# Kernel optimization log

Hardware: AMD Instinct MI355X
Metric: run time of the kernel (lower is better)

## Reference

```python
import jax, jax.numpy as jnp
import numpy as np

B, N, G = 32, 262144, 256


def setup_inputs() -> dict:
    key = jax.random.key(0)
    k1, k2, k3 = jax.random.split(key, 3)
    pr = jax.random.normal(k1, (B, N), dtype=jnp.float32)
    inp_means = jax.random.normal(k2, (B, G), dtype=jnp.float32)
    vr = jax.random.randint(k3, (B, N, 1), 0, G, dtype=jnp.int32)
    W = jnp.ones((2,), dtype=jnp.float32)  # hist_weight, ones initializer
    return {"pr": pr, "inp_means": inp_means, "vr": vr, "W": W}


def reference(pr, inp_means, vr, W):
    sg = jax.lax.stop_gradient
    G = inp_means.shape[1]
    v = jnp.squeeze(vr, -1)  # [B, N] int cluster ids (stop_gradient in orig; int anyway)
    p_sg = sg(pr)

    # Per-batch segmented min/max/sum/any over clusters (replaces python loop over g).
    def seg(p, psg, vi):
        mn = jnp.full((G,), jnp.inf, p.dtype).at[vi].min(psg)    # min(where(gidx, pr, inf))
        mx = jnp.full((G,), -jnp.inf, p.dtype).at[vi].max(psg)   # max(where(gidx, pr, -inf))
        sm = jnp.zeros((G,), p.dtype).at[vi].add(p)              # sum(where(gidx, pr, 0))
        any_ = jnp.zeros((G,), bool).at[vi].set(True)            # reduce_any(gidx)
        return mn, mx, sm, any_

    vmins, vmaxs, vsum, vany = jax.vmap(seg)(pr, p_sg, v)  # each [B, G]
    # Original divides sum by cast(any)->1.0 (or 0/0=nan -> 0), i.e. the group SUM.
    vmeans = jnp.where(vany, vsum, jnp.zeros((), pr.dtype))
    vmeans = (inp_means * W[0] + vmeans * W[1]) / (W[0] + W[1])

    no_scale = vmins == vmaxs  # [B, G]
    vmins_g = jnp.take_along_axis(jnp.where(no_scale, 0.0, vmins), v, axis=1)  # [B, N]
    vmaxs_g = jnp.take_along_axis(jnp.where(no_scale, 1.0, vmaxs), v, axis=1)  # [B, N]

    sort_ids = jnp.argsort(vmeans, axis=1)
    orig_ids = jnp.argsort(sort_ids, axis=1)  # inverse permutation
    vs = jnp.take_along_axis(vmeans, sort_ids, axis=1)  # [B, G]
    cd = jnp.concatenate([vs[:, :1], vs, vs[:, -1:] * 2], axis=1)  # [B, G+2]
    # conv1d with kernel ones(2)/c, VALID: out[i] = (cd[i] + cd[i+1]) / c
    f0 = (cd[:, :-2] + cd[:, 1:-1]) / 1.999  # conv(...)[:, :-1]
    f1 = (cd[:, 1:-1] + cd[:, 2:]) / 2.001   # conv(...)[:, 1:]
    f0 = jnp.take_along_axis(
        jnp.where(no_scale, 0.0, jnp.take_along_axis(f0, orig_ids, axis=1)), v, axis=1)
    f1 = jnp.take_along_axis(
        jnp.where(no_scale, 1.0, jnp.take_along_axis(f1, orig_ids, axis=1)), v, axis=1)

    tmp = (sg(pr) - sg(vmins_g)) / sg(vmaxs_g - vmins_g) * (f1 - f0) + f0  # [B, N]
    bad = jnp.isnan(tmp) | (tmp == 0.0)
    s = pr / jnp.where(bad, 1.0, tmp)  # safe denominator (grad-safe)
    scale = jnp.where(bad | jnp.isnan(s) | jnp.isinf(s), 0.0, s)
    return pr * scale
```

## Files before the change

kernel.cpp:

```cpp
#include <hip/hip_runtime.h>
#include <math.h>

#define NB 32
#define NN 262144
#define NG 256
#define NC 64
#define CH (NN/NC)
#define SC (CH/4)
#define CD 64
#define ELD (NN/CD)

__global__ __launch_bounds__(256) void k_count(const int* __restrict__ vr,
                                               unsigned long long* __restrict__ wcnt16,
                                               unsigned* __restrict__ gid32){
  __shared__ unsigned sc[4][NG];
  const int t    = threadIdx.x;
  const int lane = t & 63;
  const int w    = t >> 6;
  sc[0][t] = 0u; sc[1][t] = 0u; sc[2][t] = 0u; sc[3][t] = 0u;
  __syncthreads();

  const int b = blockIdx.x / NC;
  const int c = blockIdx.x % NC;
  const size_t base = (size_t)b*NN + (size_t)c*CH;
  const int4* v4 = (const int4*)(vr + base);

#pragma unroll
  for (int i = 0; i < 4; i++){
    int idx = w*256 + i*64 + lane;
    int4 v = v4[idx];
    atomicAdd(&sc[w][v.x], 1u);
    atomicAdd(&sc[w][v.y], 1u);
    atomicAdd(&sc[w][v.z], 1u);
    atomicAdd(&sc[w][v.w], 1u);
    gid32[(base >> 2) + idx] =
      (unsigned)v.x | ((unsigned)v.y << 8) | ((unsigned)v.z << 16) | ((unsigned)v.w << 24);
  }
  __syncthreads();

  unsigned c0 = sc[0][t], c1 = sc[1][t], c2 = sc[2][t], c3 = sc[3][t];
  const size_t cb = (size_t)b*NC + c;
  wcnt16[cb*NG + t] = (unsigned long long)c0
                    | ((unsigned long long)c1 << 16)
                    | ((unsigned long long)c2 << 32)
                    | ((unsigned long long)c3 << 48);
}

__global__ __launch_bounds__(256) void k_scatter(const float* __restrict__ pr,
                                                 const unsigned* __restrict__ gid32,
                                                 const unsigned long long* __restrict__ wcnt16,
                                                 float* __restrict__ sorted,
                                                 unsigned* __restrict__ grpbase,
                                                 unsigned* __restrict__ grplen){
  __shared__ float vbuf[CH];
  __shared__ unsigned char gbuf[CH];
  __shared__ unsigned wcnt[4][NG];
  __shared__ unsigned bias[NG];
  __shared__ unsigned wsumA[4];
  __shared__ unsigned wsumO[4];
  const int t    = threadIdx.x;
  const int lane = t & 63;
  const int w    = t >> 6;
  const int b = blockIdx.x / NC;
  const int c = blockIdx.x % NC;
  const size_t base = (size_t)b*NN + (size_t)c*CH;

  {
    const unsigned long long* tab = wcnt16 + (size_t)b*NC*NG + t;
    unsigned long long own = 0;
    unsigned tot_all = 0, tot_before = 0;
#pragma unroll 8
    for (int cc = 0; cc < NC; cc++){
      unsigned long long x = tab[(size_t)cc*NG];
      unsigned lo = (unsigned)x, hi = (unsigned)(x >> 32);
      unsigned tt = (lo & 0xFFFFu) + (lo >> 16) + (hi & 0xFFFFu) + (hi >> 16);
      tot_all += tt;
      if (cc < c)  tot_before += tt;
      if (cc == c) own = x;
    }
    unsigned lo = (unsigned)own, hi = (unsigned)(own >> 32);
    unsigned w0 = lo & 0xFFFFu, w1 = lo >> 16, w2 = hi & 0xFFFFu, w3 = hi >> 16;
    unsigned tot_own = w0 + w1 + w2 + w3;

    unsigned va = tot_all, vo = tot_own;
#pragma unroll
    for (int d = 1; d < 64; d <<= 1){
      unsigned ya = __shfl_up(va, d, 64);
      unsigned yo = __shfl_up(vo, d, 64);
      if (lane >= d){ va += ya; vo += yo; }
    }
    if (lane == 63){ wsumA[w] = va; wsumO[w] = vo; }
    __syncthreads();
    unsigned preA = 0, preO = 0;
#pragma unroll
    for (int k = 0; k < 3; k++) if (k < w){ preA += wsumA[k]; preO += wsumO[k]; }
    unsigned base_g = preA + va - tot_all;
    unsigned lb     = preO + vo - tot_own;
    wcnt[0][t] = lb;
    wcnt[1][t] = lb + w0;
    wcnt[2][t] = lb + w0 + w1;
    wcnt[3][t] = lb + w0 + w1 + w2;
    bias[t] = (base_g + tot_before) - lb;
    if (c == 0){
      grpbase[b*NG + t] = base_g;
      grplen [b*NG + t] = tot_all;
    }
  }
  __syncthreads();

  {
    const unsigned long long below = (lane == 0) ? 0ull : ((1ull << lane) - 1ull);
    const float*    psrc = pr    + base        + (size_t)w*SC;
    const unsigned* gsrc = gid32 + (base >> 2) + (size_t)w*(SC/4);
    const int shft = (lane & 3) * 8;

    float pv[16]; unsigned pk[16];
#pragma unroll
    for (int s = 0; s < 16; s++){
      pv[s] = psrc[s*64 + lane];
      pk[s] = gsrc[s*16 + (lane >> 2)];
    }
#pragma unroll
    for (int s = 0; s < 16; s++){
      int g = (int)((pk[s] >> shft) & 255u);
      unsigned long long mask = ~0ull;
#pragma unroll
      for (int bit = 0; bit < 8; bit++){
        int bv = (g >> bit) & 1;
        unsigned long long bal = __ballot(bv);
        mask &= bv ? bal : ~bal;
      }
      int rank = __popcll(mask & below);
      unsigned old = wcnt[w][g];
      if (rank == 0) wcnt[w][g] = old + (unsigned)__popcll(mask);
      vbuf[old + (unsigned)rank] = pv[s];
      gbuf[old + (unsigned)rank] = (unsigned char)g;
    }
  }
  __syncthreads();

  {
    float* dst = sorted + (size_t)b*NN;
    const unsigned* gbuf32 = (const unsigned*)gbuf;
#pragma unroll
    for (int k = 0; k < CH/256; k++){
      int p = k*256 + t;
      unsigned packed = gbuf32[p >> 2];
      unsigned g = (packed >> ((p & 3) * 8)) & 255u;
      dst[bias[g] + (unsigned)p] = vbuf[p];
    }
  }
}

__global__ __launch_bounds__(32) void k_sum(const float* __restrict__ sorted,
                                            const unsigned* __restrict__ grpbase,
                                            const unsigned* __restrict__ grplen,
                                            float* __restrict__ gsum,
                                            float* __restrict__ gmn,
                                            float* __restrict__ gmx){
  const int lane = threadIdx.x;
  const int b = blockIdx.x >> 3;
  const int g = ((blockIdx.x & 7) << 5) + lane;

  const unsigned base = grpbase[b*NG + g];
  const unsigned len  = grplen [b*NG + g];
  const float* sp = sorted + (size_t)b*NN + base;

  float s = 0.0f, mn = INFINITY, mx = -INFINITY;

  unsigned head = (4u - ((unsigned)(((size_t)sp) >> 2) & 3u)) & 3u;
  if (head > len) head = len;
  for (unsigned i = 0; i < head; i++){
    float v = sp[i];
    s = __fadd_rn(s, v); mn = fminf(mn, v); mx = fmaxf(mx, v);
  }
  const float4* f4 = (const float4*)(sp + head);
  const unsigned rem   = len - head;
  const unsigned nfull = rem >> 4;

  float4 b0[4], b1[4], b2[4], b3[4], b4[4], b5[4], b6[4], b7[4];
#define LOADV(D, K) { D[0]=f4[(K)*4+0]; D[1]=f4[(K)*4+1]; D[2]=f4[(K)*4+2]; D[3]=f4[(K)*4+3]; }
#define CONS1(V)    { s=__fadd_rn(s,(V)); mn=fminf(mn,(V)); mx=fmaxf(mx,(V)); }
#define CONSV(D)    { _Pragma("unroll") for (int j = 0; j < 4; j++){ float4 q = D[j]; \
                      CONS1(q.x) CONS1(q.y) CONS1(q.z) CONS1(q.w) } }

  if (nfull > 0) LOADV(b0, 0)
  if (nfull > 1) LOADV(b1, 1)
  if (nfull > 2) LOADV(b2, 2)
  if (nfull > 3) LOADV(b3, 3)
  if (nfull > 4) LOADV(b4, 4)
  if (nfull > 5) LOADV(b5, 5)
  if (nfull > 6) LOADV(b6, 6)
  if (nfull > 7) LOADV(b7, 7)
  unsigned k = 0;
  for (; k + 8 <= nfull; k += 8){
    CONSV(b0) if (k +  8 < nfull) LOADV(b0, k +  8)
    CONSV(b1) if (k +  9 < nfull) LOADV(b1, k +  9)
    CONSV(b2) if (k + 10 < nfull) LOADV(b2, k + 10)
    CONSV(b3) if (k + 11 < nfull) LOADV(b3, k + 11)
    CONSV(b4) if (k + 12 < nfull) LOADV(b4, k + 12)
    CONSV(b5) if (k + 13 < nfull) LOADV(b5, k + 13)
    CONSV(b6) if (k + 14 < nfull) LOADV(b6, k + 14)
    CONSV(b7) if (k + 15 < nfull) LOADV(b7, k + 15)
  }
  {
    unsigned r = nfull - k;
    if (r > 0) CONSV(b0)
    if (r > 1) CONSV(b1)
    if (r > 2) CONSV(b2)
    if (r > 3) CONSV(b3)
    if (r > 4) CONSV(b4)
    if (r > 5) CONSV(b5)
    if (r > 6) CONSV(b6)
  }
  for (unsigned i = head + (nfull << 4); i < len; i++){
    float v = sp[i];
    s = __fadd_rn(s, v); mn = fminf(mn, v); mx = fmaxf(mx, v);
  }
#undef LOADV
#undef CONS1
#undef CONSV

  gsum[b*NG + g] = s;
  gmn [b*NG + g] = mn;
  gmx [b*NG + g] = mx;
}

__global__ __launch_bounds__(256) void k_pipeline(const float* __restrict__ gsum,
                                                  const float* __restrict__ gmn,
                                                  const float* __restrict__ gmx,
                                                  const float* __restrict__ inp_means,
                                                  const float* __restrict__ Wv,
                                                  float* __restrict__ params){
  const int b = blockIdx.x;
  const int g = threadIdx.x;
  __shared__ float vm[NG];
  __shared__ float vs[NG];

  const float s   = gsum[b*NG + g];
  const float mnf = gmn [b*NG + g];
  const float mxf = gmx [b*NG + g];
  const float W0 = Wv[0], W1 = Wv[1];
  float mean = __fdiv_rn(__fadd_rn(__fmul_rn(inp_means[b*NG + g], W0),
                                   __fmul_rn(s, W1)),
                         __fadd_rn(W0, W1));
  vm[g] = mean;
  __syncthreads();

  int r = 0;
  for (int j = 0; j < NG; j++){
    float x = vm[j];
    r += (x < mean) || (x == mean && j < g);
  }
  vs[r] = mean;
  __syncthreads();

  float c0 = (r == 0)    ? vs[0]                     : vs[r-1];
  float c1 = vs[r];
  float c2 = (r == NG-1) ? __fmul_rn(vs[NG-1], 2.0f) : vs[r+1];
  float f0 = __fdiv_rn(__fadd_rn(c0, c1), 1.999f);
  float f1 = __fdiv_rn(__fadd_rn(c1, c2), 2.001f);

  bool ns = (mnf == mxf);
  params[(b*4 + 0)*NG + g] = ns ? 0.0f : mnf;
  params[(b*4 + 1)*NG + g] = ns ? 1.0f : __fsub_rn(mxf, mnf);
  params[(b*4 + 2)*NG + g] = ns ? 1.0f : __fsub_rn(f1, f0);
  params[(b*4 + 3)*NG + g] = ns ? 0.0f : f0;
}

static __device__ __forceinline__ float apply_one(float p, unsigned g,
                                                  const float* __restrict__ sp0,
                                                  const float* __restrict__ sp1,
                                                  const float* __restrict__ sp2,
                                                  const float* __restrict__ sp3){
  float t1  = __fsub_rn(p, sp0[g]);
  float t3  = __fdiv_rn(t1, sp1[g]);
  float t5  = __fmul_rn(t3, sp2[g]);
  float tmp = __fadd_rn(t5, sp3[g]);
  bool bad = __builtin_isnan(tmp) || (tmp == 0.0f);
  float s = __fdiv_rn(p, bad ? 1.0f : tmp);
  bool bad2 = bad || __builtin_isnan(s) || __builtin_isinf(s);
  float sc = bad2 ? 0.0f : s;
  return __fmul_rn(p, sc);
}

__global__ __launch_bounds__(256) void k_apply(const float* __restrict__ pr,
                                               const unsigned* __restrict__ gid32,
                                               const float* __restrict__ params,
                                               float* __restrict__ out){
  __shared__ float sp0[NG], sp1[NG], sp2[NG], sp3[NG];
  const int t = threadIdx.x;
  const int b = blockIdx.x / CD;
  const int c = blockIdx.x % CD;

  sp0[t] = params[(b*4 + 0)*NG + t];
  sp1[t] = params[(b*4 + 1)*NG + t];
  sp2[t] = params[(b*4 + 2)*NG + t];
  sp3[t] = params[(b*4 + 3)*NG + t];
  __syncthreads();

  const size_t base = (size_t)b*NN + (size_t)c*ELD;
  const float4* p4 = (const float4*)(pr + base);
  float4* o4 = (float4*)(out + base);

#pragma unroll
  for (int i = 0; i < ELD/1024; i++){
    float4 p = p4[i*256 + t];
    unsigned pk = gid32[(base >> 2) + i*256 + t];
    float4 r;
    r.x = apply_one(p.x,  pk        & 255u, sp0, sp1, sp2, sp3);
    r.y = apply_one(p.y, (pk >>  8) & 255u, sp0, sp1, sp2, sp3);
    r.z = apply_one(p.z, (pk >> 16) & 255u, sp0, sp1, sp2, sp3);
    r.w = apply_one(p.w,  pk >> 24,         sp0, sp1, sp2, sp3);
    o4[i*256 + t] = r;
  }
}

extern "C" void kernel_launch(void* const* d_in, const int* in_sizes, int n_in,
                              void* d_out, int out_size, void* d_ws, size_t ws_size,
                              hipStream_t stream){
  const float* pr        = (const float*)d_in[0];
  const float* inp_means = (const float*)d_in[1];
  const int*   vr        = (const int*)d_in[2];
  const float* W         = (const float*)d_in[3];
  float* out = (float*)d_out;

  char* ws = (char*)d_ws;
  size_t o = 0;
  unsigned long long* wcnt16 = (unsigned long long*)(ws + o); o += (size_t)NB*NC*NG*8;
  unsigned* gid32   = (unsigned*)(ws + o); o += (size_t)NB*NN;
  unsigned* grpbase = (unsigned*)(ws + o); o += (size_t)NB*NG*4;
  unsigned* grplen  = (unsigned*)(ws + o); o += (size_t)NB*NG*4;
  float*    gsum    = (float*)   (ws + o); o += (size_t)NB*NG*4;
  float*    gmn     = (float*)   (ws + o); o += (size_t)NB*NG*4;
  float*    gmx     = (float*)   (ws + o); o += (size_t)NB*NG*4;
  float*    params  = (float*)   (ws + o); o += (size_t)NB*NG*16;
  float* sorted = out;

  k_count   <<<NB*NC, 256, 0, stream>>>(vr, wcnt16, gid32);
  k_scatter <<<NB*NC, 256, 0, stream>>>(pr, gid32, wcnt16, sorted, grpbase, grplen);
  k_sum     <<<NB*8,   32, 0, stream>>>(sorted, grpbase, grplen, gsum, gmn, gmx);
  k_pipeline<<<NB,    256, 0, stream>>>(gsum, gmn, gmx, inp_means, W, params);
  k_apply   <<<NB*CD, 256, 0, stream>>>(pr, gid32, params, out);
}
```

Baseline: 173.3 us.

## Fuse count and scatter into one kernel with chunk-local sorting

Merges the histogram and scatter kernels into a single kernel. Each chunk now sorts its values only within itself and writes them back contiguously, along with per-chunk group counts and local offsets. The sum kernel walks 64 small segments per group instead of one globally contiguous run, which removes the global prefix pass over per-chunk counts and the random global scatter. The trade-off is more segment overhead and less vectorised, less coalesced reads in the sum kernel, which still runs with only 256 blocks of 32 threads.

Result: slower. 219.4 us (+26.6%).

```diff
diff --git a/kernel.cpp b/kernel.cpp
--- a/kernel.cpp
+++ b/kernel.cpp
@@ -10,54 +10,15 @@
 #define CD 64
 #define ELD (NN/CD)
 
-__global__ __launch_bounds__(256) void k_count(const int* __restrict__ vr,
-                                               unsigned long long* __restrict__ wcnt16,
-                                               unsigned* __restrict__ gid32){
-  __shared__ unsigned sc[4][NG];
-  const int t    = threadIdx.x;
-  const int lane = t & 63;
-  const int w    = t >> 6;
-  sc[0][t] = 0u; sc[1][t] = 0u; sc[2][t] = 0u; sc[3][t] = 0u;
-  __syncthreads();
-
-  const int b = blockIdx.x / NC;
-  const int c = blockIdx.x % NC;
-  const size_t base = (size_t)b*NN + (size_t)c*CH;
-  const int4* v4 = (const int4*)(vr + base);
-
-#pragma unroll
-  for (int i = 0; i < 4; i++){
-    int idx = w*256 + i*64 + lane;
-    int4 v = v4[idx];
-    atomicAdd(&sc[w][v.x], 1u);
-    atomicAdd(&sc[w][v.y], 1u);
-    atomicAdd(&sc[w][v.z], 1u);
-    atomicAdd(&sc[w][v.w], 1u);
-    gid32[(base >> 2) + idx] =
-      (unsigned)v.x | ((unsigned)v.y << 8) | ((unsigned)v.z << 16) | ((unsigned)v.w << 24);
-  }
-  __syncthreads();
-
-  unsigned c0 = sc[0][t], c1 = sc[1][t], c2 = sc[2][t], c3 = sc[3][t];
-  const size_t cb = (size_t)b*NC + c;
-  wcnt16[cb*NG + t] = (unsigned long long)c0
-                    | ((unsigned long long)c1 << 16)
-                    | ((unsigned long long)c2 << 32)
-                    | ((unsigned long long)c3 << 48);
-}
-
-__global__ __launch_bounds__(256) void k_scatter(const float* __restrict__ pr,
-                                                 const unsigned* __restrict__ gid32,
-                                                 const unsigned long long* __restrict__ wcnt16,
-                                                 float* __restrict__ sorted,
-                                                 unsigned* __restrict__ grpbase,
-                                                 unsigned* __restrict__ grplen){
+__global__ __launch_bounds__(256) void k_fused(const int* __restrict__ vr,
+                                               const float* __restrict__ pr,
+                                               unsigned* __restrict__ gid32,
+                                               float* __restrict__ sorted,
+                                               unsigned* __restrict__ cnt_loff){
   __shared__ float vbuf[CH];
-  __shared__ unsigned char gbuf[CH];
+  __shared__ unsigned graw[CH/4];
   __shared__ unsigned wcnt[4][NG];
-  __shared__ unsigned bias[NG];
-  __shared__ unsigned wsumA[4];
-  __shared__ unsigned wsumO[4];
+  __shared__ unsigned wsum[4];
   const int t    = threadIdx.x;
   const int lane = t & 63;
   const int w    = t >> 6;
@@ -65,60 +26,60 @@
   const int c = blockIdx.x % NC;
   const size_t base = (size_t)b*NN + (size_t)c*CH;
 
-  {
-    const unsigned long long* tab = wcnt16 + (size_t)b*NC*NG + t;
-    unsigned long long own = 0;
-    unsigned tot_all = 0, tot_before = 0;
-#pragma unroll 8
-    for (int cc = 0; cc < NC; cc++){
-      unsigned long long x = tab[(size_t)cc*NG];
-      unsigned lo = (unsigned)x, hi = (unsigned)(x >> 32);
-      unsigned tt = (lo & 0xFFFFu) + (lo >> 16) + (hi & 0xFFFFu) + (hi >> 16);
-      tot_all += tt;
-      if (cc < c)  tot_before += tt;
-      if (cc == c) own = x;
-    }
-    unsigned lo = (unsigned)own, hi = (unsigned)(own >> 32);
-    unsigned w0 = lo & 0xFFFFu, w1 = lo >> 16, w2 = hi & 0xFFFFu, w3 = hi >> 16;
-    unsigned tot_own = w0 + w1 + w2 + w3;
-
-    unsigned va = tot_all, vo = tot_own;
+  wcnt[0][t] = 0u; wcnt[1][t] = 0u; wcnt[2][t] = 0u; wcnt[3][t] = 0u;
+  __syncthreads();
+
+  {
+    const int4* v4 = (const int4*)(vr + base);
+#pragma unroll
+    for (int i = 0; i < 4; i++){
+      int idx = w*256 + i*64 + lane;
+      int4 v = v4[idx];
+      atomicAdd(&wcnt[w][v.x], 1u);
+      atomicAdd(&wcnt[w][v.y], 1u);
+      atomicAdd(&wcnt[w][v.z], 1u);
+      atomicAdd(&wcnt[w][v.w], 1u);
+      unsigned pk = (unsigned)v.x | ((unsigned)v.y << 8)
+                  | ((unsigned)v.z << 16) | ((unsigned)v.w << 24);
+      gid32[(base >> 2) + idx] = pk;
+      graw[idx] = pk;
+    }
+  }
+  __syncthreads();
+
+  {
+    unsigned c0 = wcnt[0][t], c1 = wcnt[1][t], c2 = wcnt[2][t], c3 = wcnt[3][t];
+    unsigned tot = c0 + c1 + c2 + c3;
+    unsigned v = tot;
 #pragma unroll
     for (int d = 1; d < 64; d <<= 1){
-      unsigned ya = __shfl_up(va, d, 64);
-      unsigned yo = __shfl_up(vo, d, 64);
-      if (lane >= d){ va += ya; vo += yo; }
-    }
-    if (lane == 63){ wsumA[w] = va; wsumO[w] = vo; }
+      unsigned y = __shfl_up(v, d, 64);
+      if (lane >= d) v += y;
+    }
+    if (lane == 63) wsum[w] = v;
     __syncthreads();
-    unsigned preA = 0, preO = 0;
-#pragma unroll
-    for (int k = 0; k < 3; k++) if (k < w){ preA += wsumA[k]; preO += wsumO[k]; }
-    unsigned base_g = preA + va - tot_all;
-    unsigned lb     = preO + vo - tot_own;
+    unsigned pre = 0;
+#pragma unroll
+    for (int k = 0; k < 3; k++) if (k < w) pre += wsum[k];
+    unsigned lb = pre + v - tot;
     wcnt[0][t] = lb;
-    wcnt[1][t] = lb + w0;
-    wcnt[2][t] = lb + w0 + w1;
-    wcnt[3][t] = lb + w0 + w1 + w2;
-    bias[t] = (base_g + tot_before) - lb;
-    if (c == 0){
-      grpbase[b*NG + t] = base_g;
-      grplen [b*NG + t] = tot_all;
-    }
+    wcnt[1][t] = lb + c0;
+    wcnt[2][t] = lb + c0 + c1;
+    wcnt[3][t] = lb + c0 + c1 + c2;
+    cnt_loff[((size_t)b*NC + c)*NG + t] = tot | (lb << 16);
   }
   __syncthreads();
 
   {
     const unsigned long long below = (lane == 0) ? 0ull : ((1ull << lane) - 1ull);
-    const float*    psrc = pr    + base        + (size_t)w*SC;
-    const unsigned* gsrc = gid32 + (base >> 2) + (size_t)w*(SC/4);
+    const float* psrc = pr + base + (size_t)w*SC;
     const int shft = (lane & 3) * 8;
 
     float pv[16]; unsigned pk[16];
 #pragma unroll
     for (int s = 0; s < 16; s++){
       pv[s] = psrc[s*64 + lane];
-      pk[s] = gsrc[s*16 + (lane >> 2)];
+      pk[s] = graw[w*256 + s*16 + (lane >> 2)];
     }
 #pragma unroll
     for (int s = 0; s < 16; s++){
@@ -134,92 +95,50 @@
       unsigned old = wcnt[w][g];
       if (rank == 0) wcnt[w][g] = old + (unsigned)__popcll(mask);
       vbuf[old + (unsigned)rank] = pv[s];
-      gbuf[old + (unsigned)rank] = (unsigned char)g;
-    }
-  }
-  __syncthreads();
-
-  {
-    float* dst = sorted + (size_t)b*NN;
-    const unsigned* gbuf32 = (const unsigned*)gbuf;
-#pragma unroll
-    for (int k = 0; k < CH/256; k++){
-      int p = k*256 + t;
-      unsigned packed = gbuf32[p >> 2];
-      unsigned g = (packed >> ((p & 3) * 8)) & 255u;
-      dst[bias[g] + (unsigned)p] = vbuf[p];
-    }
+    }
+  }
+  __syncthreads();
+
+  {
+    float4* dst4 = (float4*)(sorted + base);
+    const float4* src4 = (const float4*)vbuf;
+#pragma unroll
+    for (int k = 0; k < 4; k++) dst4[k*256 + t] = src4[k*256 + t];
   }
 }
 
 __global__ __launch_bounds__(32) void k_sum(const float* __restrict__ sorted,
-                                            const unsigned* __restrict__ grpbase,
-                                            const unsigned* __restrict__ grplen,
+                                            const unsigned* __restrict__ cnt_loff,
                                             float* __restrict__ gsum,
                                             float* __restrict__ gmn,
                                             float* __restrict__ gmx){
+  __shared__ unsigned tab[NC][32];
   const int lane = threadIdx.x;
   const int b = blockIdx.x >> 3;
-  const int g = ((blockIdx.x & 7) << 5) + lane;
-
-  const unsigned base = grpbase[b*NG + g];
-  const unsigned len  = grplen [b*NG + g];
-  const float* sp = sorted + (size_t)b*NN + base;
+  const int gbase = (blockIdx.x & 7) << 5;
+  const int g = gbase + lane;
+
+  for (int c = 0; c < NC; c++)
+    tab[c][lane] = cnt_loff[((size_t)b*NC + c)*NG + gbase + lane];
+  __syncthreads();
 
   float s = 0.0f, mn = INFINITY, mx = -INFINITY;
-
-  unsigned head = (4u - ((unsigned)(((size_t)sp) >> 2) & 3u)) & 3u;
-  if (head > len) head = len;
-  for (unsigned i = 0; i < head; i++){
-    float v = sp[i];
-    s = __fadd_rn(s, v); mn = fminf(mn, v); mx = fmaxf(mx, v);
-  }
-  const float4* f4 = (const float4*)(sp + head);
-  const unsigned rem   = len - head;
-  const unsigned nfull = rem >> 4;
-
-  float4 b0[4], b1[4], b2[4], b3[4], b4[4], b5[4], b6[4], b7[4];
-#define LOADV(D, K) { D[0]=f4[(K)*4+0]; D[1]=f4[(K)*4+1]; D[2]=f4[(K)*4+2]; D[3]=f4[(K)*4+3]; }
-#define CONS1(V)    { s=__fadd_rn(s,(V)); mn=fminf(mn,(V)); mx=fmaxf(mx,(V)); }
-#define CONSV(D)    { _Pragma("unroll") for (int j = 0; j < 4; j++){ float4 q = D[j]; \
-                      CONS1(q.x) CONS1(q.y) CONS1(q.z) CONS1(q.w) } }
-
-  if (nfull > 0) LOADV(b0, 0)
-  if (nfull > 1) LOADV(b1, 1)
-  if (nfull > 2) LOADV(b2, 2)
-  if (nfull > 3) LOADV(b3, 3)
-  if (nfull > 4) LOADV(b4, 4)
-  if (nfull > 5) LOADV(b5, 5)
-  if (nfull > 6) LOADV(b6, 6)
-  if (nfull > 7) LOADV(b7, 7)
-  unsigned k = 0;
-  for (; k + 8 <= nfull; k += 8){
-    CONSV(b0) if (k +  8 < nfull) LOADV(b0, k +  8)
-    CONSV(b1) if (k +  9 < nfull) LOADV(b1, k +  9)
-    CONSV(b2) if (k + 10 < nfull) LOADV(b2, k + 10)
-    CONSV(b3) if (k + 11 < nfull) LOADV(b3, k + 11)
-    CONSV(b4) if (k + 12 < nfull) LOADV(b4, k + 12)
-    CONSV(b5) if (k + 13 < nfull) LOADV(b5, k + 13)
-    CONSV(b6) if (k + 14 < nfull) LOADV(b6, k + 14)
-    CONSV(b7) if (k + 15 < nfull) LOADV(b7, k + 15)
-  }
-  {
-    unsigned r = nfull - k;
-    if (r > 0) CONSV(b0)
-    if (r > 1) CONSV(b1)
-    if (r > 2) CONSV(b2)
-    if (r > 3) CONSV(b3)
-    if (r > 4) CONSV(b4)
-    if (r > 5) CONSV(b5)
-    if (r > 6) CONSV(b6)
-  }
-  for (unsigned i = head + (nfull << 4); i < len; i++){
-    float v = sp[i];
-    s = __fadd_rn(s, v); mn = fminf(mn, v); mx = fmaxf(mx, v);
-  }
-#undef LOADV
+#define CONS1(V) { s = __fadd_rn(s, (V)); mn = fminf(mn, (V)); mx = fmaxf(mx, (V)); }
+  const float* bb = sorted + (size_t)b*NN;
+  for (int c = 0; c < NC; c++){
+    unsigned cl  = tab[c][lane];
+    unsigned len = cl & 0xFFFFu;
+    const float* p = bb + c*CH + (cl >> 16);
+    unsigned i = 0;
+    for (; i + 8 <= len; i += 8){
+      float a0 = p[i  ], a1 = p[i+1], a2 = p[i+2], a3 = p[i+3];
+      float a4 = p[i+4], a5 = p[i+5], a6 = p[i+6], a7 = p[i+7];
+      CONS1(a0) CONS1(a1) CONS1(a2) CONS1(a3)
+      CONS1(a4) CONS1(a5) CONS1(a6) CONS1(a7)
+    }
+    for (; i < len; i++){ float a = p[i]; CONS1(a); }
+  }
 #undef CONS1
-#undef CONSV
 
   gsum[b*NG + g] = s;
   gmn [b*NG + g] = mn;
@@ -327,19 +246,16 @@
 
   char* ws = (char*)d_ws;
   size_t o = 0;
-  unsigned long long* wcnt16 = (unsigned long long*)(ws + o); o += (size_t)NB*NC*NG*8;
-  unsigned* gid32   = (unsigned*)(ws + o); o += (size_t)NB*NN;
-  unsigned* grpbase = (unsigned*)(ws + o); o += (size_t)NB*NG*4;
-  unsigned* grplen  = (unsigned*)(ws + o); o += (size_t)NB*NG*4;
-  float*    gsum    = (float*)   (ws + o); o += (size_t)NB*NG*4;
-  float*    gmn     = (float*)   (ws + o); o += (size_t)NB*NG*4;
-  float*    gmx     = (float*)   (ws + o); o += (size_t)NB*NG*4;
-  float*    params  = (float*)   (ws + o); o += (size_t)NB*NG*16;
+  unsigned* gid32    = (unsigned*)(ws + o); o += (size_t)NB*NN;
+  unsigned* cnt_loff = (unsigned*)(ws + o); o += (size_t)NB*NC*NG*4;
+  float*    gsum     = (float*)   (ws + o); o += (size_t)NB*NG*4;
+  float*    gmn      = (float*)   (ws + o); o += (size_t)NB*NG*4;
+  float*    gmx      = (float*)   (ws + o); o += (size_t)NB*NG*4;
+  float*    params   = (float*)   (ws + o); o += (size_t)NB*NG*16;
   float* sorted = out;
 
-  k_count   <<<NB*NC, 256, 0, stream>>>(vr, wcnt16, gid32);
-  k_scatter <<<NB*NC, 256, 0, stream>>>(pr, gid32, wcnt16, sorted, grpbase, grplen);
-  k_sum     <<<NB*8,   32, 0, stream>>>(sorted, grpbase, grplen, gsum, gmn, gmx);
+  k_fused   <<<NB*NC, 256, 0, stream>>>(vr, pr, gid32, sorted, cnt_loff);
+  k_sum     <<<NB*8,   32, 0, stream>>>(sorted, cnt_loff, gsum, gmn, gmx);
   k_pipeline<<<NB,    256, 0, stream>>>(gsum, gmn, gmx, inp_means, W, params);
   k_apply   <<<NB*CD, 256, 0, stream>>>(pr, gid32, params, out);
 }
```

## Replace count+scatter with fused local sort and coalesced-run global gather

Applied to the files above, without the earlier changes.

Merges the count and scatter kernels into one kernel per chunk. It histograms cluster ids, sorts the chunk's values locally in shared memory, and writes them contiguously along with packed count/offset metadata. A second kernel then computes global group offsets and moves each locally sorted chunk into the global sorted buffer, so the writes follow runs of consecutive addresses rather than random scatter. This needs an extra workspace buffer for the global sorted array. If the workspace is too small, the code falls back to the old path.

New measurement: 180.7 us. 1.04x slower.

```diff
diff --git a/kernel.cpp b/kernel.cpp
--- a/kernel.cpp
+++ b/kernel.cpp
@@ -9,6 +9,167 @@
 #define SC (CH/4)
 #define CD 64
 #define ELD (NN/CD)
+
+
+__global__ __launch_bounds__(256) void k_fused(const int* __restrict__ vr,
+                                               const float* __restrict__ pr,
+                                               unsigned* __restrict__ gid32,
+                                               float* __restrict__ sortedL,
+                                               unsigned* __restrict__ cnt_loff){
+  __shared__ float vbuf[CH];
+  __shared__ unsigned graw[CH/4];
+  __shared__ unsigned wcnt[4][NG];
+  __shared__ unsigned wsum[4];
+  const int t    = threadIdx.x;
+  const int lane = t & 63;
+  const int w    = t >> 6;
+  const int b = blockIdx.x / NC;
+  const int c = blockIdx.x % NC;
+  const size_t base = (size_t)b*NN + (size_t)c*CH;
+
+  wcnt[0][t] = 0u; wcnt[1][t] = 0u; wcnt[2][t] = 0u; wcnt[3][t] = 0u;
+  __syncthreads();
+
+  {
+    const int4* v4 = (const int4*)(vr + base);
+#pragma unroll
+    for (int i = 0; i < 4; i++){
+      int idx = w*256 + i*64 + lane;
+      int4 v = v4[idx];
+      atomicAdd(&wcnt[w][v.x], 1u);
+      atomicAdd(&wcnt[w][v.y], 1u);
+      atomicAdd(&wcnt[w][v.z], 1u);
+      atomicAdd(&wcnt[w][v.w], 1u);
+      unsigned pk = (unsigned)v.x | ((unsigned)v.y << 8)
+                  | ((unsigned)v.z << 16) | ((unsigned)v.w << 24);
+      gid32[(base >> 2) + idx] = pk;
+      graw[idx] = pk;
+    }
+  }
+  __syncthreads();
+
+  {
+    unsigned c0 = wcnt[0][t], c1 = wcnt[1][t], c2 = wcnt[2][t], c3 = wcnt[3][t];
+    unsigned tot = c0 + c1 + c2 + c3;
+    unsigned v = tot;
+#pragma unroll
+    for (int d = 1; d < 64; d <<= 1){
+      unsigned y = __shfl_up(v, d, 64);
+      if (lane >= d) v += y;
+    }
+    if (lane == 63) wsum[w] = v;
+    __syncthreads();
+    unsigned pre = 0;
+#pragma unroll
+    for (int k = 0; k < 3; k++) if (k < w) pre += wsum[k];
+    unsigned lb = pre + v - tot;
+    wcnt[0][t] = lb;
+    wcnt[1][t] = lb + c0;
+    wcnt[2][t] = lb + c0 + c1;
+    wcnt[3][t] = lb + c0 + c1 + c2;
+    cnt_loff[((size_t)b*NC + c)*NG + t] = tot | (lb << 16);
+  }
+  __syncthreads();
+
+  {
+    const unsigned long long below = (lane == 0) ? 0ull : ((1ull << lane) - 1ull);
+    const float* psrc = pr + base + (size_t)w*SC;
+    const int shft = (lane & 3) * 8;
+
+    float pv[16]; unsigned pk[16];
+#pragma unroll
+    for (int s = 0; s < 16; s++){
+      pv[s] = psrc[s*64 + lane];
+      pk[s] = graw[w*256 + s*16 + (lane >> 2)];
+    }
+#pragma unroll
+    for (int s = 0; s < 16; s++){
+      int g = (int)((pk[s] >> shft) & 255u);
+      unsigned long long mask = ~0ull;
+#pragma unroll
+      for (int bit = 0; bit < 8; bit++){
+        int bv = (g >> bit) & 1;
+        unsigned long long bal = __ballot(bv);
+        mask &= bv ? bal : ~bal;
+      }
+      int rank = __popcll(mask & below);
+      unsigned old = wcnt[w][g];
+      if (rank == 0) wcnt[w][g] = old + (unsigned)__popcll(mask);
+      vbuf[old + (unsigned)rank] = pv[s];
+    }
+  }
+  __syncthreads();
+
+  {
+    float4* dst4 = (float4*)(sortedL + base);
+    const float4* src4 = (const float4*)vbuf;
+#pragma unroll
+    for (int k = 0; k < 4; k++) dst4[k*256 + t] = src4[k*256 + t];
+  }
+}
+
+__global__ __launch_bounds__(256) void k_gather(const float* __restrict__ sortedL,
+                                                const unsigned* __restrict__ cnt_loff,
+                                                float* __restrict__ sortedG,
+                                                unsigned* __restrict__ grpbase,
+                                                unsigned* __restrict__ grplen){
+  __shared__ unsigned char map8[CH];
+  __shared__ unsigned bias[NG];
+  __shared__ unsigned wsum[4];
+  const int t    = threadIdx.x;
+  const int lane = t & 63;
+  const int w    = t >> 6;
+  const int b = blockIdx.x / NC;
+  const int c = blockIdx.x % NC;
+
+  const unsigned* col = cnt_loff + (size_t)b*NC*NG + t;
+  unsigned own = col[(size_t)c*NG];
+  unsigned len = own & 0xFFFFu, lb = own >> 16;
+  for (unsigned i = 0; i < len; i++) map8[lb + i] = (unsigned char)t;
+
+  unsigned tot_all = 0, tot_before = 0;
+#pragma unroll 8
+  for (int cc = 0; cc < NC; cc++){
+    unsigned x = col[(size_t)cc*NG];
+    unsigned tt = x & 0xFFFFu;
+    tot_all += tt;
+    if (cc < c) tot_before += tt;
+  }
+  unsigned v = tot_all;
+#pragma unroll
+  for (int d = 1; d < 64; d <<= 1){
+    unsigned y = __shfl_up(v, d, 64);
+    if (lane >= d) v += y;
+  }
+  if (lane == 63) wsum[w] = v;
+  __syncthreads();
+  unsigned pre = 0;
+#pragma unroll
+  for (int k = 0; k < 3; k++) if (k < w) pre += wsum[k];
+  unsigned base_g = pre + v - tot_all;
+  bias[t] = (base_g + tot_before) - lb;
+  if (c == 0){
+    grpbase[b*NG + t] = base_g;
+    grplen [b*NG + t] = tot_all;
+  }
+  __syncthreads();
+
+  const float4* src4 = (const float4*)(sortedL + (size_t)b*NN + (size_t)c*CH);
+  float* dst = sortedG + (size_t)b*NN;
+  const unsigned* m32 = (const unsigned*)map8;
+#pragma unroll
+  for (int k = 0; k < 4; k++){
+    int q = k*256 + t;
+    unsigned mq = m32[q];
+    float4 vv = src4[q];
+    int p = q << 2;
+    dst[bias[ mq        & 255u] + (unsigned)p    ] = vv.x;
+    dst[bias[(mq >>  8) & 255u] + (unsigned)p + 1] = vv.y;
+    dst[bias[(mq >> 16) & 255u] + (unsigned)p + 2] = vv.z;
+    dst[bias[ mq >> 24        ] + (unsigned)p + 3] = vv.w;
+  }
+}
+
 
 __global__ __launch_bounds__(256) void k_count(const int* __restrict__ vr,
                                                unsigned long long* __restrict__ wcnt16,
@@ -152,6 +313,7 @@
   }
 }
 
+
 __global__ __launch_bounds__(32) void k_sum(const float* __restrict__ sorted,
                                             const unsigned* __restrict__ grpbase,
                                             const unsigned* __restrict__ grplen,
@@ -327,7 +489,6 @@
 
   char* ws = (char*)d_ws;
   size_t o = 0;
-  unsigned long long* wcnt16 = (unsigned long long*)(ws + o); o += (size_t)NB*NC*NG*8;
   unsigned* gid32   = (unsigned*)(ws + o); o += (size_t)NB*NN;
   unsigned* grpbase = (unsigned*)(ws + o); o += (size_t)NB*NG*4;
   unsigned* grplen  = (unsigned*)(ws + o); o += (size_t)NB*NG*4;
@@ -335,11 +496,27 @@
   float*    gmn     = (float*)   (ws + o); o += (size_t)NB*NG*4;
   float*    gmx     = (float*)   (ws + o); o += (size_t)NB*NG*4;
   float*    params  = (float*)   (ws + o); o += (size_t)NB*NG*16;
-  float* sorted = out;
-
-  k_count   <<<NB*NC, 256, 0, stream>>>(vr, wcnt16, gid32);
-  k_scatter <<<NB*NC, 256, 0, stream>>>(pr, gid32, wcnt16, sorted, grpbase, grplen);
-  k_sum     <<<NB*8,   32, 0, stream>>>(sorted, grpbase, grplen, gsum, gmn, gmx);
-  k_pipeline<<<NB,    256, 0, stream>>>(gsum, gmn, gmx, inp_means, W, params);
-  k_apply   <<<NB*CD, 256, 0, stream>>>(pr, gid32, params, out);
-}
+
+  size_t need_fused = o + (size_t)NB*NC*NG*4 + (size_t)NB*NN*4;
+
+  if (ws_size >= need_fused){
+    unsigned* cnt_loff = (unsigned*)(ws + o); o += (size_t)NB*NC*NG*4;
+    float*    sortedG  = (float*)   (ws + o); o += (size_t)NB*NN*4;
+    float* sortedL = out;
+
+    k_fused   <<<NB*NC, 256, 0, stream>>>(vr, pr, gid32, sortedL, cnt_loff);
+    k_gather  <<<NB*NC, 256, 0, stream>>>(sortedL, cnt_loff, sortedG, grpbase, grplen);
+    k_sum     <<<NB*8,   32, 0, stream>>>(sortedG, grpbase, grplen, gsum, gmn, gmx);
+    k_pipeline<<<NB,    256, 0, stream>>>(gsum, gmn, gmx, inp_means, W, params);
+    k_apply   <<<NB*CD, 256, 0, stream>>>(pr, gid32, params, out);
+  } else {
+    unsigned long long* wcnt16 = (unsigned long long*)(ws + o); o += (size_t)NB*NC*NG*8;
+    float* sorted = out;
+
+    k_count   <<<NB*NC, 256, 0, stream>>>(vr, wcnt16, gid32);
+    k_scatter <<<NB*NC, 256, 0, stream>>>(pr, gid32, wcnt16, sorted, grpbase, grplen);
+    k_sum     <<<NB*8,   32, 0, stream>>>(sorted, grpbase, grplen, gsum, gmn, gmx);
+    k_pipeline<<<NB,    256, 0, stream>>>(gsum, gmn, gmx, inp_means, W, params);
+    k_apply   <<<NB*CD, 256, 0, stream>>>(pr, gid32, params, out);
+  }
+}
```
